# Optimization experiments

Hardware: AMD Instinct MI355X
Metric: run time of the kernel (lower is better)

Reference implementation:

```python
import jax, jax.numpy as jnp
import numpy as np

HID = 256; NH = 8; DH = 32; NL = 2
NV = 20000; NT = 50000; NE = 100000; NC = 8; FIN = 64


def setup_inputs() -> dict:
    ks = jax.random.split(jax.random.key(0), 32)
    f = lambda i, sh, s: jax.random.normal(ks[i], sh, dtype=jnp.float32) * s
    return {
        "x_v": f(0, (NV, FIN), 1.0),
        "x_t": f(1, (NT, FIN), 1.0),
        "ei_vt_src": jax.random.randint(ks[2], (NE,), 0, NV),
        "ei_vt_dst": jax.random.randint(ks[3], (NE,), 0, NT),
        "ei_tv_src": jax.random.randint(ks[4], (NE,), 0, NT),
        "ei_tv_dst": jax.random.randint(ks[5], (NE,), 0, NV),
        "ei_tt_src": jax.random.randint(ks[6], (NE,), 0, NT),
        "ei_tt_dst": jax.random.randint(ks[7], (NE,), 0, NT),
        "current": jax.random.randint(ks[8], (NC, 2), 0, NV),
        "W_in_v": f(9, (FIN, HID), 0.05), "b_in_v": jnp.zeros((HID,)),
        "W_in_t": f(10, (FIN, HID), 0.05), "b_in_t": jnp.zeros((HID,)),
        "Wk": f(11, (NL, 2, HID, HID), 0.05), "bk": jnp.zeros((NL, 2, HID)),
        "Wq": f(12, (NL, 2, HID, HID), 0.05), "bq": jnp.zeros((NL, 2, HID)),
        "Wv": f(13, (NL, 2, HID, HID), 0.05), "bv": jnp.zeros((NL, 2, HID)),
        "Wa": f(14, (NL, 2, HID, HID), 0.05), "ba": jnp.zeros((NL, 2, HID)),
        "skip": jnp.zeros((NL, 2)),
        "a_rel": f(15, (NL, 3, NH, DH, DH), 0.1),
        "m_rel": f(16, (NL, 3, NH, DH, DH), 0.1),
        "p_rel": jnp.ones((NL, 3, NH)),
        "Ws1": f(17, (2 * HID, HID), 0.05), "bs1": jnp.zeros((HID,)),
        "Ws2": f(18, (HID, 2), 0.05), "bs2": jnp.zeros((2,)),
    }


def reference(x_v, x_t, ei_vt_src, ei_vt_dst, ei_tv_src, ei_tv_dst,
              ei_tt_src, ei_tt_dst, current,
              W_in_v, b_in_v, W_in_t, b_in_t,
              Wk, bk, Wq, bq, Wv, bv, Wa, ba, skip,
              a_rel, m_rel, p_rel, Ws1, bs1, Ws2, bs2):
    scale = 1.0 / jnp.sqrt(jnp.float32(DH))
    # input projections + relu (lin_dict)
    hv = jax.nn.relu(x_v @ W_in_v + b_in_v)
    ht = jax.nn.relu(x_t @ W_in_t + b_in_t)
    # edge types: (src_type, dst_type, rel_idx, src_idx, dst_idx); 0=vehicle, 1=track
    edges = [(0, 1, 0, ei_vt_src, ei_vt_dst),
             (1, 0, 1, ei_tv_src, ei_tv_dst),
             (1, 1, 2, ei_tt_src, ei_tt_dst)]
    for l in range(NL):
        h = (hv, ht)
        proj = lambda W, b, t: (h[t] @ W[l, t] + b[l, t]).reshape(-1, NH, DH)
        k = (proj(Wk, bk, 0), proj(Wk, bk, 1))
        q = (proj(Wq, bq, 0), proj(Wq, bq, 1))
        v = (proj(Wv, bv, 0), proj(Wv, bv, 1))
        agg = [jnp.zeros((NV, NH, DH), jnp.float32),
               jnp.zeros((NT, NH, DH), jnp.float32)]
        for (st, dt, r, si, di) in edges:
            nd = agg[dt].shape[0]
            ke = jnp.einsum('ehd,hdf->ehf', k[st][si], a_rel[l, r])  # [E,H,D]
            ve = jnp.einsum('ehd,hdf->ehf', v[st][si], m_rel[l, r])  # [E,H,D]
            logit = (q[dt][di] * ke).sum(-1) * p_rel[l, r] * scale    # [E,H]
            m = jax.ops.segment_max(logit, di, num_segments=nd)
            e = jnp.exp(logit - m[di])
            s = jax.ops.segment_sum(e, di, num_segments=nd)
            alpha = e / (s[di] + 1e-16)
            agg[dt] = agg[dt] + jax.ops.segment_sum(alpha[..., None] * ve, di,
                                                    num_segments=nd)
        new = []
        for t in (0, 1):
            o = jax.nn.gelu(agg[t].reshape(-1, HID), approximate=False) @ Wa[l, t] + ba[l, t]
            beta = jax.nn.sigmoid(skip[l, t])
            new.append(beta * o + (1.0 - beta) * h[t])
        hv, ht = new
    # batched Scorer over (current vehicles) x (all tracks); cat([track, vehicle])
    veh = hv[current[:, 0]]                 # [C,HID]
    tpart = ht @ Ws1[:HID]                  # [NT,HID]
    vpart = veh @ Ws1[HID:] + bs1           # [C,HID]
    hmid = jax.nn.relu(tpart[None, :, :] + vpart[:, None, :])  # [C,NT,HID]
    out = hmid @ Ws2 + bs2                  # [C,NT,2]
    return out[..., 0], jax.nn.sigmoid(out[..., 1])
```

## Files before the change

kernel.cpp:

```cpp
#include <hip/hip_runtime.h>
#include <hip/hip_bf16.h>
#include <math.h>

#define HID 256
#define NH 8
#define DH 32
#define NL 2
#define NV 20000
#define NT 50000
#define NE 100000
#define NC 8
#define FIN 64

typedef unsigned short u16;
typedef unsigned int u32;
typedef short s16x8 __attribute__((ext_vector_type(8)));
typedef float f32x4 __attribute__((ext_vector_type(4)));

__device__ __forceinline__ float bf2f(u16 u) { return __uint_as_float(((u32)u) << 16); }
__device__ __forceinline__ u16 f2bf(float f) {
    u32 x = __float_as_uint(f);
    u32 r = ((x >> 16) & 1u) + 0x7fffu;
    return (u16)((x + r) >> 16);
}
__device__ __forceinline__ void up2(u32 u, float& a, float& b) {
    a = __uint_as_float(u << 16);
    b = __uint_as_float(u & 0xffff0000u);
}
__device__ __forceinline__ s16x8 gelu8(s16x8 a) {
    s16x8 r;
#pragma unroll
    for (int i = 0; i < 8; i++) {
        float v = bf2f((u16)a[i]);
        v = 0.5f * v * (1.f + erff(v * 0.70710678118654752f));
        r[i] = (short)f2bf(v);
    }
    return r;
}

__global__ void k_zero_i(int* __restrict__ p, int n) {
    for (int i = blockIdx.x * 256 + threadIdx.x; i < n; i += gridDim.x * 256) p[i] = 0;
}

__global__ void k_hist3(const int* __restrict__ d0, const int* __restrict__ d1, const int* __restrict__ d2,
                        int* __restrict__ cnt3) {
    int r = blockIdx.x >> 9;
    int b = blockIdx.x & 511;
    const int* dst = (r == 0) ? d0 : (r == 1) ? d1 : d2;
    int* cnt = cnt3 + (size_t)r * NT;
    for (int e = b * 256 + threadIdx.x; e < NE; e += 512 * 256)
        atomicAdd(&cnt[dst[e]], 1);
}

__global__ __launch_bounds__(1024) void k_scan3(const int* __restrict__ cnt3,
                                                int* __restrict__ rp0, int* __restrict__ rp1, int* __restrict__ rp2) {
    int r = blockIdx.x;
    const int* cnt = cnt3 + (size_t)r * NT;
    int* rp = (r == 0) ? rp0 : (r == 1) ? rp1 : rp2;
    int n = (r == 1) ? NV : NT;
    __shared__ int wsum[16];
    __shared__ int carry_s;
    int t = threadIdx.x, lane = t & 63, wv = t >> 6;
    if (t == 0) { carry_s = 0; rp[0] = 0; }
    __syncthreads();
    for (int base = 0; base < n; base += 1024) {
        int v = (base + t < n) ? cnt[base + t] : 0;
        int x = v;
#pragma unroll
        for (int off = 1; off < 64; off <<= 1) {
            int y = __shfl_up(x, off, 64);
            if (lane >= off) x += y;
        }
        if (lane == 63) wsum[wv] = x;
        __syncthreads();
        if (wv == 0 && lane < 16) {
            int s = wsum[lane];
#pragma unroll
            for (int off = 1; off < 16; off <<= 1) {
                int y = __shfl_up(s, off, 64);
                if (lane >= off) s += y;
            }
            wsum[lane] = s;
        }
        __syncthreads();
        int prefix = carry_s + (wv > 0 ? wsum[wv - 1] : 0);
        if (base + t < n) rp[base + t + 1] = prefix + x;
        __syncthreads();
        if (t == 0) carry_s += wsum[15];
        __syncthreads();
    }
}

__global__ void k_copy3(const int* __restrict__ rp0, const int* __restrict__ rp1, const int* __restrict__ rp2,
                        int* __restrict__ fill3) {
    int r = blockIdx.x >> 8;
    int b = blockIdx.x & 255;
    const int* rp = (r == 0) ? rp0 : (r == 1) ? rp1 : rp2;
    int n = (r == 1) ? NV : NT;
    int* fill = fill3 + (size_t)r * NT;
    for (int i = b * 256 + threadIdx.x; i < n; i += 256 * 256) fill[i] = rp[i];
}

__global__ void k_scatter3(const int* __restrict__ d0, const int* __restrict__ s0,
                           const int* __restrict__ d1, const int* __restrict__ s1,
                           const int* __restrict__ d2, const int* __restrict__ s2,
                           int* __restrict__ fill3,
                           int* __restrict__ es0, int* __restrict__ es1, int* __restrict__ es2) {
    int r = blockIdx.x >> 9;
    int b = blockIdx.x & 511;
    const int* dst = (r == 0) ? d0 : (r == 1) ? d1 : d2;
    const int* src = (r == 0) ? s0 : (r == 1) ? s1 : s2;
    int* fill = fill3 + (size_t)r * NT;
    int* es = (r == 0) ? es0 : (r == 1) ? es1 : es2;
    for (int e = b * 256 + threadIdx.x; e < NE; e += 512 * 256) {
        int d = dst[e];
        int p = atomicAdd(&fill[d], 1);
        es[p] = src[e];
    }
}

__global__ __launch_bounds__(256) void k_in_proj(const float* __restrict__ X, const float* __restrict__ W,
                          const float* __restrict__ b, u16* __restrict__ Y, int N) {
    const int NPB = 16;
    __shared__ float xs[NPB][FIN];
    int n0 = blockIdx.x * NPB;
    int t = threadIdx.x;
    for (int idx = t; idx < NPB * FIN; idx += 256) {
        int i = idx >> 6, c = idx & 63;
        int n = n0 + i;
        xs[i][c] = (n < N) ? X[(size_t)n * FIN + c] : 0.f;
    }
    __syncthreads();
    float acc[NPB];
#pragma unroll
    for (int i = 0; i < NPB; i++) acc[i] = 0.f;
    for (int c = 0; c < FIN; c++) {
        float w = W[c * HID + t];
#pragma unroll
        for (int i = 0; i < NPB; i++) acc[i] += xs[i][c] * w;
    }
    float bb = b[t];
    for (int i = 0; i < NPB; i++) {
        int n = n0 + i;
        if (n < N) Y[(size_t)n * HID + t] = f2bf(fmaxf(acc[i] + bb, 0.f));
    }
}

__device__ __forceinline__ int swz_idx(int k, int n) {
    int ks = k >> 5, r = k & 31;
    int j = r & 7;
    int l = ((r >> 3) << 4) | (n & 15);
    int nt = n >> 4;
    return ((ks * 16 + nt) * 64 + l) * 8 + j;
}

__global__ __launch_bounds__(256) void k_fuse_w2(
        const float* __restrict__ Wk_, const float* __restrict__ bk_, const float* __restrict__ Rk,
        u16* __restrict__ WswK, float* __restrict__ bkO,
        const float* __restrict__ Wv_, const float* __restrict__ bv_, const float* __restrict__ Rv,
        u16* __restrict__ WswV, float* __restrict__ bvO) {
    int h = blockIdx.x & 7;
    int which = blockIdx.x >> 3;
    const float* W = which ? Wv_ : Wk_;
    const float* b = which ? bv_ : bk_;
    const float* R = which ? Rv : Rk;
    u16* Wsw = which ? WswV : WswK;
    float* bout = which ? bvO : bkO;
    __shared__ float sR[DH * DH];
    int t = threadIdx.x;
    for (int idx = t; idx < DH * DH; idx += 256) sR[idx] = R[h * DH * DH + idx];
    __syncthreads();
    int f = t & 31, c0 = t >> 5;
    for (int c = c0; c < HID; c += 8) {
        float acc = 0.f;
#pragma unroll
        for (int d = 0; d < DH; d++) acc += W[c * HID + h * DH + d] * sR[d * DH + f];
        Wsw[swz_idx(c, h * DH + f)] = f2bf(acc);
    }
    if (t < DH) {
        float acc = 0.f;
#pragma unroll
        for (int d = 0; d < DH; d++) acc += b[h * DH + d] * sR[d * DH + t];
        bout[h * DH + t] = acc;
    }
}

__global__ __launch_bounds__(256) void k_swz_multi(const float* __restrict__ Wq, const float* __restrict__ Wa,
                                                   const float* __restrict__ Ws1, u16* __restrict__ out) {
    int slot = blockIdx.x >> 8;
    int idx = ((blockIdx.x & 255) << 8) | threadIdx.x;
    const float* src = (slot < 4) ? (Wq + (size_t)slot * 65536)
                     : (slot < 8) ? (Wa + (size_t)(slot - 4) * 65536)
                                  : Ws1;
    int j = idx & 7, l = (idx >> 3) & 63, nt = (idx >> 9) & 15, ks = idx >> 13;
    int k = ks * 32 + (l >> 4) * 8 + j;
    int n = nt * 16 + (l & 15);
    out[(size_t)slot * 65536 + idx] = f2bf(src[k * HID + n]);
}

template <int MODE, int GELU>
__global__ __launch_bounds__(256) void k_mm(const u16* __restrict__ X, const u16* __restrict__ Wsw,
                                            const float* __restrict__ bias, void* __restrict__ Y,
                                            const float* __restrict__ skip_, int N) {
    int tid = threadIdx.x;
    int w = tid >> 6, lane = tid & 63;
    int r0 = blockIdx.x * 16;
    int rA = r0 + (lane & 15);
    int koffg = lane >> 4;
    s16x8 a[8];
    if (rA < N) {
        const s16x8* ap = (const s16x8*)(X + (size_t)rA * HID) + koffg;
#pragma unroll
        for (int ks = 0; ks < 8; ks++) a[ks] = ap[ks * 4];
    } else {
#pragma unroll
        for (int ks = 0; ks < 8; ks++) a[ks] = (s16x8){0, 0, 0, 0, 0, 0, 0, 0};
    }
    if (GELU) {
#pragma unroll
        for (int ks = 0; ks < 8; ks++) a[ks] = gelu8(a[ks]);
    }
    f32x4 acc[4];
#pragma unroll
    for (int nt = 0; nt < 4; nt++) acc[nt] = (f32x4){0.f, 0.f, 0.f, 0.f};
    const s16x8* wp = (const s16x8*)Wsw;
#pragma unroll
    for (int ks = 0; ks < 8; ks++) {
        const s16x8* wq = wp + (size_t)ks * 16 * 64 + lane;
#pragma unroll
        for (int nt = 0; nt < 4; nt++) {
            s16x8 b = wq[(w * 4 + nt) * 64];
            acc[nt] = __builtin_amdgcn_mfma_f32_16x16x32_bf16(a[ks], b, acc[nt], 0, 0, 0);
        }
    }
    int colb = lane & 15;
    int rowb = r0 + koffg * 4;
    float beta = 0.f, ombeta = 0.f;
    if (MODE == 2) { beta = 1.f / (1.f + expf(-skip_[0])); ombeta = 1.f - beta; }
#pragma unroll
    for (int nt = 0; nt < 4; nt++) {
        int col = w * 64 + nt * 16 + colb;
        float bb = (MODE == 1 || MODE == 3) ? 0.f : bias[col];
#pragma unroll
        for (int j = 0; j < 4; j++) {
            int row = rowb + j;
            if (row < N) {
                float v = acc[nt][j] + bb;
                if (MODE == 0 || MODE == 3) {
                    ((u16*)Y)[(size_t)row * HID + col] = f2bf(v);
                } else if (MODE == 1) {
                    ((float*)Y)[(size_t)row * HID + col] = v;
                } else {
                    u16* hp = (u16*)Y + (size_t)row * HID + col;
                    *hp = f2bf(beta * v + ombeta * bf2f(*hp));
                }
            }
        }
    }
}

__global__ __launch_bounds__(256) void k_mm_gt(const u16* __restrict__ agg, const u16* __restrict__ WaSw,
                                               const float* __restrict__ ba_, const float* __restrict__ skip_,
                                               const u16* __restrict__ ht_old, const u16* __restrict__ Ws1Sw,
                                               u16* __restrict__ tpart, int N) {
    __shared__ u16 sH[16][264];
    int tid = threadIdx.x;
    int w = tid >> 6, lane = tid & 63;
    int r0 = blockIdx.x * 16;
    int rA = r0 + (lane & 15);
    int koffg = lane >> 4;
    s16x8 a[8];
    {
        const s16x8* ap = (const s16x8*)(agg + (size_t)rA * HID) + koffg;
#pragma unroll
        for (int ks = 0; ks < 8; ks++) a[ks] = gelu8(ap[ks * 4]);
    }
    f32x4 acc[4];
#pragma unroll
    for (int nt = 0; nt < 4; nt++) acc[nt] = (f32x4){0.f, 0.f, 0.f, 0.f};
    const s16x8* wp = (const s16x8*)WaSw;
#pragma unroll
    for (int ks = 0; ks < 8; ks++) {
        const s16x8* wq = wp + (size_t)ks * 16 * 64 + lane;
#pragma unroll
        for (int nt = 0; nt < 4; nt++)
            acc[nt] = __builtin_amdgcn_mfma_f32_16x16x32_bf16(a[ks], wq[(w * 4 + nt) * 64], acc[nt], 0, 0, 0);
    }
    float beta = 1.f / (1.f + expf(-skip_[0])), ombeta = 1.f - beta;
    int colb = lane & 15;
    int rowl = koffg * 4;
#pragma unroll
    for (int nt = 0; nt < 4; nt++) {
        int col = w * 64 + nt * 16 + colb;
        float bb = ba_[col];
#pragma unroll
        for (int j = 0; j < 4; j++) {
            int row = r0 + rowl + j;
            float v = acc[nt][j] + bb;
            float o = beta * v + ombeta * bf2f(ht_old[(size_t)row * HID + col]);
            sH[rowl + j][col] = f2bf(o);
        }
    }
    __syncthreads();
    s16x8 a2[8];
#pragma unroll
    for (int ks = 0; ks < 8; ks++)
        a2[ks] = *(const s16x8*)&sH[lane & 15][ks * 32 + koffg * 8];
#pragma unroll
    for (int nt = 0; nt < 4; nt++) acc[nt] = (f32x4){0.f, 0.f, 0.f, 0.f};
    const s16x8* wp2 = (const s16x8*)Ws1Sw;
#pragma unroll
    for (int ks = 0; ks < 8; ks++) {
        const s16x8* wq = wp2 + (size_t)ks * 16 * 64 + lane;
#pragma unroll
        for (int nt = 0; nt < 4; nt++)
            acc[nt] = __builtin_amdgcn_mfma_f32_16x16x32_bf16(a2[ks], wq[(w * 4 + nt) * 64], acc[nt], 0, 0, 0);
    }
#pragma unroll
    for (int nt = 0; nt < 4; nt++) {
        int col = w * 64 + nt * 16 + colb;
#pragma unroll
        for (int j = 0; j < 4; j++) {
            int row = r0 + rowl + j;
            if (row < N) tpart[(size_t)row * HID + col] = f2bf(acc[nt][j]);
        }
    }
}

__global__ __launch_bounds__(256) void k_mm2(const u16* __restrict__ X,
                                             const u16* __restrict__ W1, const float* __restrict__ b1, u16* __restrict__ Y1,
                                             const u16* __restrict__ W2, const float* __restrict__ b2, u16* __restrict__ Y2,
                                             int N) {
    int tid = threadIdx.x;
    int w = tid >> 6, lane = tid & 63;
    int r0 = blockIdx.x * 16;
    int rA = r0 + (lane & 15);
    int koffg = lane >> 4;
    s16x8 a[8];
    if (rA < N) {
        const s16x8* ap = (const s16x8*)(X + (size_t)rA * HID) + koffg;
#pragma unroll
        for (int ks = 0; ks < 8; ks++) a[ks] = ap[ks * 4];
    } else {
#pragma unroll
        for (int ks = 0; ks < 8; ks++) a[ks] = (s16x8){0, 0, 0, 0, 0, 0, 0, 0};
    }
    int colb = lane & 15;
    int rowb = r0 + koffg * 4;
#pragma unroll
    for (int pass = 0; pass < 2; pass++) {
        const u16* Wsw = pass ? W2 : W1;
        const float* bias = pass ? b2 : b1;
        u16* Y = pass ? Y2 : Y1;
        f32x4 acc[4];
#pragma unroll
        for (int nt = 0; nt < 4; nt++) acc[nt] = (f32x4){0.f, 0.f, 0.f, 0.f};
        const s16x8* wp = (const s16x8*)Wsw;
#pragma unroll
        for (int ks = 0; ks < 8; ks++) {
            const s16x8* wq = wp + (size_t)ks * 16 * 64 + lane;
#pragma unroll
            for (int nt = 0; nt < 4; nt++) {
                s16x8 b = wq[(w * 4 + nt) * 64];
                acc[nt] = __builtin_amdgcn_mfma_f32_16x16x32_bf16(a[ks], b, acc[nt], 0, 0, 0);
            }
        }
#pragma unroll
        for (int nt = 0; nt < 4; nt++) {
            int col = w * 64 + nt * 16 + colb;
            float bb = bias[col];
#pragma unroll
            for (int j = 0; j < 4; j++) {
                int row = rowb + j;
                if (row < N) Y[(size_t)row * HID + col] = f2bf(acc[nt][j] + bb);
            }
        }
    }
}

__global__ __launch_bounds__(256) void k_mm3(const u16* __restrict__ X,
                                             const u16* __restrict__ W0, const float* __restrict__ b0, u16* __restrict__ Y0,
                                             const u16* __restrict__ W1, const float* __restrict__ b1, u16* __restrict__ Y1,
                                             const u16* __restrict__ W2, const float* __restrict__ b2, u16* __restrict__ Y2,
                                             int N) {
    int tid = threadIdx.x;
    int w = tid >> 6, lane = tid & 63;
    int r0 = blockIdx.x * 16;
    int rA = r0 + (lane & 15);
    int koffg = lane >> 4;
    s16x8 a[8];
    if (rA < N) {
        const s16x8* ap = (const s16x8*)(X + (size_t)rA * HID) + koffg;
#pragma unroll
        for (int ks = 0; ks < 8; ks++) a[ks] = ap[ks * 4];
    } else {
#pragma unroll
        for (int ks = 0; ks < 8; ks++) a[ks] = (s16x8){0, 0, 0, 0, 0, 0, 0, 0};
    }
    int colb = lane & 15;
    int rowb = r0 + koffg * 4;
#pragma unroll
    for (int pass = 0; pass < 3; pass++) {
        const u16* Wsw = (pass == 0) ? W0 : (pass == 1) ? W1 : W2;
        const float* bias = (pass == 0) ? b0 : (pass == 1) ? b1 : b2;
        u16* Y = (pass == 0) ? Y0 : (pass == 1) ? Y1 : Y2;
        f32x4 acc[4];
#pragma unroll
        for (int nt = 0; nt < 4; nt++) acc[nt] = (f32x4){0.f, 0.f, 0.f, 0.f};
        const s16x8* wp = (const s16x8*)Wsw;
#pragma unroll
        for (int ks = 0; ks < 8; ks++) {
            const s16x8* wq = wp + (size_t)ks * 16 * 64 + lane;
#pragma unroll
            for (int nt = 0; nt < 4; nt++) {
                s16x8 b = wq[(w * 4 + nt) * 64];
                acc[nt] = __builtin_amdgcn_mfma_f32_16x16x32_bf16(a[ks], b, acc[nt], 0, 0, 0);
            }
        }
#pragma unroll
        for (int nt = 0; nt < 4; nt++) {
            int col = w * 64 + nt * 16 + colb;
            float bb = bias[col];
#pragma unroll
            for (int j = 0; j < 4; j++) {
                int row = rowb + j;
                if (row < N) Y[(size_t)row * HID + col] = f2bf(acc[nt][j] + bb);
            }
        }
    }
}

__device__ __forceinline__ void attn_pass(const u16* __restrict__ kA, const u16* __restrict__ vM,
                                          const int* __restrict__ es, int jb, int je,
                                          float q0, float q1, float q2, float q3, float ph, int lane4,
                                          float& o0, float& o1, float& o2, float& o3) {
    float m = -INFINITY, ss = 0.f, a0 = 0.f, a1 = 0.f, a2 = 0.f, a3 = 0.f;
    uint2 ku0 = {0, 0}, vu0 = {0, 0}, ku1 = {0, 0}, vu1 = {0, 0};
    if (jb < je) {
        int s = es[jb];
        ku0 = *(const uint2*)(kA + (size_t)s * HID + lane4);
        vu0 = *(const uint2*)(vM + (size_t)s * HID + lane4);
    }
    if (jb + 1 < je) {
        int s = es[jb + 1];
        ku1 = *(const uint2*)(kA + (size_t)s * HID + lane4);
        vu1 = *(const uint2*)(vM + (size_t)s * HID + lane4);
    }
    for (int j = jb; j < je; j++) {
        uint2 ku = ku0, vu = vu0;
        ku0 = ku1; vu0 = vu1;
        if (j + 2 < je) {
            int s = es[j + 2];
            ku1 = *(const uint2*)(kA + (size_t)s * HID + lane4);
            vu1 = *(const uint2*)(vM + (size_t)s * HID + lane4);
        }
        float k0, k1, k2, k3; up2(ku.x, k0, k1); up2(ku.y, k2, k3);
        float part = q0 * k0 + q1 * k1 + q2 * k2 + q3 * k3;
        part += __shfl_xor(part, 1, 64);
        part += __shfl_xor(part, 2, 64);
        part += __shfl_xor(part, 4, 64);
        float logit = part * ph;
        float nm = fmaxf(m, logit);
        float corr = expf(m - nm);
        float ee = expf(logit - nm);
        float v0, v1, v2, v3; up2(vu.x, v0, v1); up2(vu.y, v2, v3);
        ss = ss * corr + ee;
        a0 = a0 * corr + ee * v0; a1 = a1 * corr + ee * v1;
        a2 = a2 * corr + ee * v2; a3 = a3 * corr + ee * v3;
        m = nm;
    }
    float inv = 1.f / (ss + 1e-16f);
    o0 += a0 * inv; o1 += a1 * inv; o2 += a2 * inv; o3 += a3 * inv;
}

__global__ __launch_bounds__(256) void k_node_attn(
        const u16* __restrict__ q, const u16* __restrict__ kA, const u16* __restrict__ vM,
        const int* __restrict__ rp, const int* __restrict__ es,
        const float* __restrict__ P, float scale,
        u16* __restrict__ agg, int Nd) {
    int node = blockIdx.x * 4 + (threadIdx.x >> 6);
    if (node >= Nd) return;
    int lane = threadIdx.x & 63;
    float ph = P[lane >> 3] * scale;
    uint2 qu = *(const uint2*)(q + (size_t)node * HID + lane * 4);
    float q0, q1, q2, q3; up2(qu.x, q0, q1); up2(qu.y, q2, q3);
    float o0 = 0.f, o1 = 0.f, o2 = 0.f, o3 = 0.f;
    attn_pass(kA, vM, es, rp[node], rp[node + 1], q0, q1, q2, q3, ph, lane * 4, o0, o1, o2, o3);
    u16* ap = agg + (size_t)node * HID + lane * 4;
    ap[0] = f2bf(o0); ap[1] = f2bf(o1); ap[2] = f2bf(o2); ap[3] = f2bf(o3);
}

__global__ __launch_bounds__(256) void k_attn8(
        const u16* __restrict__ q8, const u16* __restrict__ kA, const u16* __restrict__ vM,
        const int* __restrict__ rp, const int* __restrict__ es, const int* __restrict__ current,
        const float* __restrict__ P, float scale, u16* __restrict__ agg8) {
    int wv = blockIdx.x * 4 + (threadIdx.x >> 6);
    if (wv >= NC) return;
    int node = current[wv * 2];
    int lane = threadIdx.x & 63;
    int lane4 = lane * 4;
    float ph = P[lane >> 3] * scale;
    uint2 qu = *(const uint2*)(q8 + (size_t)wv * HID + lane4);
    float q0, q1, q2, q3; up2(qu.x, q0, q1); up2(qu.y, q2, q3);
    float o0 = 0.f, o1 = 0.f, o2 = 0.f, o3 = 0.f;
    attn_pass(kA, vM, es, rp[node], rp[node + 1], q0, q1, q2, q3, ph, lane4, o0, o1, o2, o3);
    u16* ap = agg8 + (size_t)wv * HID + lane4;
    ap[0] = f2bf(o0); ap[1] = f2bf(o1); ap[2] = f2bf(o2); ap[3] = f2bf(o3);
}

__global__ __launch_bounds__(256) void k_q8(const u16* __restrict__ hv, const int* __restrict__ current,
                                            const float* __restrict__ Wq_, const float* __restrict__ bq_,
                                            u16* __restrict__ q8) {
    __shared__ float row[HID];
    int t = threadIdx.x;
    for (int c = 0; c < NC; c++) {
        int n = current[c * 2];
        row[t] = bf2f(hv[(size_t)n * HID + t]);
        __syncthreads();
        float acc = 0.f;
        for (int i = 0; i < HID; i++) acc += row[i] * Wq_[i * HID + t];
        q8[c * HID + t] = f2bf(acc + bq_[t]);
        __syncthreads();
    }
}

__global__ __launch_bounds__(256) void k_node_attn2(
        const u16* __restrict__ q,
        const u16* __restrict__ kA0, const u16* __restrict__ vM0,
        const int* __restrict__ rp0, const int* __restrict__ es0, const float* __restrict__ P0,
        const u16* __restrict__ kA1, const u16* __restrict__ vM1,
        const int* __restrict__ rp1, const int* __restrict__ es1, const float* __restrict__ P1,
        float scale, u16* __restrict__ agg, int Nd) {
    int node = blockIdx.x * 4 + (threadIdx.x >> 6);
    if (node >= Nd) return;
    int lane = threadIdx.x & 63;
    int h = lane >> 3;
    int lane4 = lane * 4;
    float ph0 = P0[h] * scale, ph1 = P1[h] * scale;
    uint2 qu = *(const uint2*)(q + (size_t)node * HID + lane4);
    float q0, q1, q2, q3; up2(qu.x, q0, q1); up2(qu.y, q2, q3);
    float o0 = 0.f, o1 = 0.f, o2 = 0.f, o3 = 0.f;
    attn_pass(kA0, vM0, es0, rp0[node], rp0[node + 1], q0, q1, q2, q3, ph0, lane4, o0, o1, o2, o3);
    attn_pass(kA1, vM1, es1, rp1[node], rp1[node + 1], q0, q1, q2, q3, ph1, lane4, o0, o1, o2, o3);
    u16* ap = agg + (size_t)node * HID + lane4;
    ap[0] = f2bf(o0); ap[1] = f2bf(o1); ap[2] = f2bf(o2); ap[3] = f2bf(o3);
}

__global__ __launch_bounds__(256) void k_vpart_f(
        const u16* __restrict__ agg8, const float* __restrict__ Wa_, const float* __restrict__ ba_,
        const float* __restrict__ skip_, const u16* __restrict__ hv, const int* __restrict__ current,
        const float* __restrict__ Ws1, const float* __restrict__ bs1, float* __restrict__ vpart) {
    __shared__ float sG[NC][HID];
    int t = threadIdx.x;
#pragma unroll
    for (int c = 0; c < NC; c++) {
        float x = bf2f(agg8[c * HID + t]);
        sG[c][t] = 0.5f * x * (1.f + erff(x * 0.70710678118654752f));
    }
    __syncthreads();
    float acc[NC];
#pragma unroll
    for (int c = 0; c < NC; c++) acc[c] = 0.f;
    for (int i = 0; i < HID; i++) {
        float wv_ = Wa_[i * HID + t];
#pragma unroll
        for (int c = 0; c < NC; c++) acc[c] += sG[c][i] * wv_;
    }
    float beta = 1.f / (1.f + expf(-skip_[0])), ombeta = 1.f - beta;
    float bb = ba_[t];
    __syncthreads();
#pragma unroll
    for (int c = 0; c < NC; c++) {
        int n = current[c * 2];
        float o = beta * (acc[c] + bb) + ombeta * bf2f(hv[(size_t)n * HID + t]);
        sG[c][t] = bf2f(f2bf(o));
    }
    __syncthreads();
    float acc2[NC];
#pragma unroll
    for (int c = 0; c < NC; c++) acc2[c] = 0.f;
    for (int i = 0; i < HID; i++) {
        float w1 = Ws1[(size_t)(HID + i) * HID + t];
#pragma unroll
        for (int c = 0; c < NC; c++) acc2[c] += sG[c][i] * w1;
    }
    float bs = bs1[t];
#pragma unroll
    for (int c = 0; c < NC; c++) vpart[c * HID + t] = acc2[c] + bs;
}

__global__ __launch_bounds__(256) void k_final(const u16* __restrict__ tpart, const float* __restrict__ vpart,
                        const float* __restrict__ Ws2, const float* __restrict__ bs2,
                        float* __restrict__ out) {
    __shared__ float vp[NC * HID];
    int t = threadIdx.x;
    for (int idx = t; idx < NC * HID; idx += 256) vp[idx] = vpart[idx];
    __syncthreads();
    int lane = t & 63, w = t >> 6;
    float w20[4], w21[4];
#pragma unroll
    for (int i = 0; i < 4; i++) {
        w20[i] = Ws2[(lane + 64 * i) * 2 + 0];
        w21[i] = Ws2[(lane + 64 * i) * 2 + 1];
    }
    float b0 = bs2[0], b1 = bs2[1];
    for (int n = blockIdx.x * 4 + w; n < NT; n += gridDim.x * 4) {
        float tp[4];
#pragma unroll
        for (int i = 0; i < 4; i++) tp[i] = bf2f(tpart[(size_t)n * HID + lane + 64 * i]);
#pragma unroll
        for (int c = 0; c < NC; c++) {
            float a0 = 0.f, a1 = 0.f;
#pragma unroll
            for (int i = 0; i < 4; i++) {
                float hm = fmaxf(tp[i] + vp[c * HID + lane + 64 * i], 0.f);
                a0 += hm * w20[i];
                a1 += hm * w21[i];
            }
#pragma unroll
            for (int off = 32; off >= 1; off >>= 1) {
                a0 += __shfl_xor(a0, off, 64);
                a1 += __shfl_xor(a1, off, 64);
            }
            if (lane == 0) {
                out[(size_t)c * NT + n] = a0 + b0;
                float z = a1 + b1;
                out[(size_t)NC * NT + (size_t)c * NT + n] = 1.f / (1.f + expf(-z));
            }
        }
    }
}

extern "C" void kernel_launch(void* const* d_in, const int* in_sizes, int n_in,
                              void* d_out, int out_size, void* d_ws, size_t ws_size,
                              hipStream_t stream) {
    (void)in_sizes; (void)n_in; (void)out_size;
    const float* x_v    = (const float*)d_in[0];
    const float* x_t    = (const float*)d_in[1];
    const int* ei_vt_s  = (const int*)d_in[2];
    const int* ei_vt_d  = (const int*)d_in[3];
    const int* ei_tv_s  = (const int*)d_in[4];
    const int* ei_tv_d  = (const int*)d_in[5];
    const int* ei_tt_s  = (const int*)d_in[6];
    const int* ei_tt_d  = (const int*)d_in[7];
    const int* current  = (const int*)d_in[8];
    const float* W_in_v = (const float*)d_in[9];
    const float* b_in_v = (const float*)d_in[10];
    const float* W_in_t = (const float*)d_in[11];
    const float* b_in_t = (const float*)d_in[12];
    const float* Wk     = (const float*)d_in[13];
    const float* bk     = (const float*)d_in[14];
    const float* Wq     = (const float*)d_in[15];
    const float* bq     = (const float*)d_in[16];
    const float* Wv     = (const float*)d_in[17];
    const float* bv     = (const float*)d_in[18];
    const float* Wa     = (const float*)d_in[19];
    const float* ba     = (const float*)d_in[20];
    const float* skip   = (const float*)d_in[21];
    const float* a_rel  = (const float*)d_in[22];
    const float* m_rel  = (const float*)d_in[23];
    const float* p_rel  = (const float*)d_in[24];
    const float* Ws1    = (const float*)d_in[25];
    const float* bs1    = (const float*)d_in[26];
    const float* Ws2    = (const float*)d_in[27];
    const float* bs2    = (const float*)d_in[28];

    char* p = (char*)d_ws;
    auto alloc = [&](size_t bytes) -> char* {
        char* r = p;
        p += (bytes + 255) & ~(size_t)255;
        return r;
    };
    u16* hv   = (u16*)alloc((size_t)NV * HID * 2);
    u16* ht   = (u16*)alloc((size_t)NT * HID * 2);
    u16* qb   = (u16*)alloc((size_t)NT * HID * 2);
    u16* qv   = (u16*)alloc((size_t)NV * HID * 2);
    u16* kA   = (u16*)alloc((size_t)NT * HID * 2);
    u16* vM   = (u16*)alloc((size_t)NT * HID * 2);
    u16* kA0  = (u16*)alloc((size_t)NV * HID * 2);
    u16* vM0  = (u16*)alloc((size_t)NV * HID * 2);
    u16* agg  = (u16*)alloc((size_t)NT * HID * 2);
    int* rp_vt = (int*)alloc((size_t)(NT + 1) * 4);
    int* rp_tv = (int*)alloc((size_t)(NV + 1) * 4);
    int* rp_tt = (int*)alloc((size_t)(NT + 1) * 4);
    int* es_vt = (int*)alloc((size_t)NE * 4);
    int* es_tv = (int*)alloc((size_t)NE * 4);
    int* es_tt = (int*)alloc((size_t)NE * 4);
    int* cnt3  = (int*)alloc((size_t)3 * NT * 4);
    int* fill3 = (int*)alloc((size_t)3 * NT * 4);
    float* vp  = (float*)alloc((size_t)NC * HID * 4);
    u16* q8   = (u16*)alloc((size_t)NC * HID * 2);
    u16* agg8 = (u16*)alloc((size_t)NC * HID * 2);
    float* bkF = (float*)alloc(HID * 4);
    float* bvF = (float*)alloc(HID * 4);
    u16*  wswK = (u16*)alloc((size_t)HID * HID * 2);
    u16*  wswV = (u16*)alloc((size_t)HID * HID * 2);
    u16*  wswK2 = (u16*)alloc((size_t)HID * HID * 2);
    u16*  wswV2 = (u16*)alloc((size_t)HID * HID * 2);
    float* bkF2 = (float*)alloc(HID * 4);
    float* bvF2 = (float*)alloc(HID * 4);
    u16*  wswA = (u16*)alloc((size_t)9 * HID * HID * 2);
    if ((size_t)(p - (char*)d_ws) > ws_size) return;

    const float scale = 0.17677669529663687f;

    k_zero_i<<<256, 256, 0, stream>>>(cnt3, 3 * NT);
    k_hist3<<<3 * 512, 256, 0, stream>>>(ei_vt_d, ei_tv_d, ei_tt_d, cnt3);
    k_scan3<<<3, 1024, 0, stream>>>(cnt3, rp_vt, rp_tv, rp_tt);
    k_copy3<<<3 * 256, 256, 0, stream>>>(rp_vt, rp_tv, rp_tt, fill3);
    k_scatter3<<<3 * 512, 256, 0, stream>>>(ei_vt_d, ei_vt_s, ei_tv_d, ei_tv_s, ei_tt_d, ei_tt_s,
                                            fill3, es_vt, es_tv, es_tt);

    k_swz_multi<<<9 * 256, 256, 0, stream>>>(Wq, Wa, Ws1, wswA);

    k_in_proj<<<(NV + 15) / 16, 256, 0, stream>>>(x_v, W_in_v, b_in_v, hv, NV);
    k_in_proj<<<(NT + 15) / 16, 256, 0, stream>>>(x_t, W_in_t, b_in_t, ht, NT);

    const int GV = (NV + 15) / 16, GT = (NT + 15) / 16;

    for (int l = 0; l < NL; l++) {
        const float* Wk0 = Wk + (size_t)(l * 2 + 0) * HID * HID;
        const float* Wk1 = Wk + (size_t)(l * 2 + 1) * HID * HID;
        const float* bk0 = bk + (l * 2 + 0) * HID, *bk1 = bk + (l * 2 + 1) * HID;
        const float* Wv0 = Wv + (size_t)(l * 2 + 0) * HID * HID;
        const float* Wv1 = Wv + (size_t)(l * 2 + 1) * HID * HID;
        const float* bv0 = bv + (l * 2 + 0) * HID, *bv1 = bv + (l * 2 + 1) * HID;
        const float* bq0 = bq + (l * 2 + 0) * HID, *bq1 = bq + (l * 2 + 1) * HID;
        const u16* WqS0 = wswA + (size_t)(l * 2 + 0) * 65536;
        const u16* WqS1 = wswA + (size_t)(l * 2 + 1) * 65536;
        const u16* WaS0 = wswA + (size_t)(4 + l * 2 + 0) * 65536;
        const u16* WaS1 = wswA + (size_t)(4 + l * 2 + 1) * 65536;
        const float* A0 = a_rel + (size_t)(l * 3 + 0) * NH * DH * DH;
        const float* A1 = a_rel + (size_t)(l * 3 + 1) * NH * DH * DH;
        const float* A2 = a_rel + (size_t)(l * 3 + 2) * NH * DH * DH;
        const float* M0 = m_rel + (size_t)(l * 3 + 0) * NH * DH * DH;
        const float* M1 = m_rel + (size_t)(l * 3 + 1) * NH * DH * DH;
        const float* M2 = m_rel + (size_t)(l * 3 + 2) * NH * DH * DH;
        const float* P0 = p_rel + (size_t)(l * 3 + 0) * NH;
        const float* P1 = p_rel + (size_t)(l * 3 + 1) * NH;
        const float* P2 = p_rel + (size_t)(l * 3 + 2) * NH;

        k_fuse_w2<<<2 * NH, 256, 0, stream>>>(Wk0, bk0, A0, wswK, bkF, Wv0, bv0, M0, wswV, bvF);
        if (l == 0) {
            k_mm3<<<GV, 256, 0, stream>>>(hv, WqS0, bq0, qv, wswK, bkF, kA0, wswV, bvF, vM0, NV);
        } else {
            k_mm2<<<GV, 256, 0, stream>>>(hv, wswK, bkF, kA0, wswV, bvF, vM0, NV);
            k_q8<<<1, 256, 0, stream>>>(hv, current, Wq + (size_t)(l * 2 + 0) * HID * HID, bq0, q8);
        }

        k_fuse_w2<<<2 * NH, 256, 0, stream>>>(Wk1, bk1, A1, wswK, bkF, Wv1, bv1, M1, wswV, bvF);
        k_mm3<<<GT, 256, 0, stream>>>(ht, WqS1, bq1, qb, wswK, bkF, kA, wswV, bvF, vM, NT);

        if (l == 0) {
            k_node_attn<<<(NV + 3) / 4, 256, 0, stream>>>(qv, kA, vM, rp_tv, es_tv, P1, scale, agg, NV);
            k_mm<2, 1><<<GV, 256, 0, stream>>>(agg, WaS0, ba + (l * 2 + 0) * HID, hv, skip + (l * 2 + 0), NV);
        } else {
            k_attn8<<<2, 256, 0, stream>>>(q8, kA, vM, rp_tv, es_tv, current, P1, scale, agg8);
        }

        k_fuse_w2<<<2 * NH, 256, 0, stream>>>(Wk1, bk1, A2, wswK2, bkF2, Wv1, bv1, M2, wswV2, bvF2);
        k_mm2<<<GT, 256, 0, stream>>>(ht, wswK2, bkF2, kA, wswV2, bvF2, vM, NT);

        k_node_attn2<<<(NT + 3) / 4, 256, 0, stream>>>(qb, kA0, vM0, rp_vt, es_vt, P0,
                                                       kA, vM, rp_tt, es_tt, P2, scale, agg, NT);

        if (l == 0) {
            k_mm<2, 1><<<GT, 256, 0, stream>>>(agg, WaS1, ba + (l * 2 + 1) * HID, ht, skip + (l * 2 + 1), NT);
        } else {
            k_mm_gt<<<GT, 256, 0, stream>>>(agg, WaS1, ba + (l * 2 + 1) * HID, skip + (l * 2 + 1),
                                            ht, wswA + (size_t)8 * 65536, kA, NT);
        }
    }

    k_vpart_f<<<1, 256, 0, stream>>>(agg8, Wa + (size_t)2 * 65536, ba + 2 * HID, skip + 2,
                                     hv, current, Ws1, bs1, vp);
    k_final<<<2048, 256, 0, stream>>>(kA , vp, Ws2, bs2, (float*)d_out);
}
```

Before: 976.9 us.

## Fuse layer-0 vehicle output projection with layer-1 K/V projection

Unrolls the layer loop and adds a kernel that applies GELU, the Wa output projection and the skip blend to the vehicle aggregate. It then reuses the updated hidden rows from shared memory to compute the next layer's K and V projections. The layer-0 vehicle attention writes into the q buffer in place, and its output projection is deferred so it merges with the layer-1 K/V matmul. This removes one kernel launch and one global round trip of hv. The risk is that reusing the qv buffer for aggregates and reordering the launches changes data dependencies.

```diff
diff --git a/kernel.cpp b/kernel.cpp
--- a/kernel.cpp
+++ b/kernel.cpp
@@ -323,6 +323,84 @@
         for (int j = 0; j < 4; j++) {
             int row = r0 + rowl + j;
             if (row < N) tpart[(size_t)row * HID + col] = f2bf(acc[nt][j]);
+        }
+    }
+}
+
+__global__ __launch_bounds__(256) void k_mm_dv(const u16* __restrict__ aggv, const u16* __restrict__ WaSw,
+                                               const float* __restrict__ ba_, const float* __restrict__ skip_,
+                                               u16* __restrict__ hv,
+                                               const u16* __restrict__ WkSw, const float* __restrict__ bkF,
+                                               const u16* __restrict__ WvSw, const float* __restrict__ bvF,
+                                               u16* __restrict__ kA0, u16* __restrict__ vM0, int N) {
+    __shared__ u16 sH[16][264];
+    int tid = threadIdx.x;
+    int w = tid >> 6, lane = tid & 63;
+    int r0 = blockIdx.x * 16;
+    int rA = r0 + (lane & 15);
+    int koffg = lane >> 4;
+    s16x8 a[8];
+    {
+        const s16x8* ap = (const s16x8*)(aggv + (size_t)rA * HID) + koffg;
+#pragma unroll
+        for (int ks = 0; ks < 8; ks++) a[ks] = gelu8(ap[ks * 4]);
+    }
+    f32x4 acc[4];
+#pragma unroll
+    for (int nt = 0; nt < 4; nt++) acc[nt] = (f32x4){0.f, 0.f, 0.f, 0.f};
+    const s16x8* wp = (const s16x8*)WaSw;
+#pragma unroll
+    for (int ks = 0; ks < 8; ks++) {
+        const s16x8* wq = wp + (size_t)ks * 16 * 64 + lane;
+#pragma unroll
+        for (int nt = 0; nt < 4; nt++)
+            acc[nt] = __builtin_amdgcn_mfma_f32_16x16x32_bf16(a[ks], wq[(w * 4 + nt) * 64], acc[nt], 0, 0, 0);
+    }
+    float beta = 1.f / (1.f + expf(-skip_[0])), ombeta = 1.f - beta;
+    int colb = lane & 15;
+    int rowl = koffg * 4;
+#pragma unroll
+    for (int nt = 0; nt < 4; nt++) {
+        int col = w * 64 + nt * 16 + colb;
+        float bb = ba_[col];
+#pragma unroll
+        for (int j = 0; j < 4; j++) {
+            int row = r0 + rowl + j;
+            float v = acc[nt][j] + bb;
+            u16 o = f2bf(beta * v + ombeta * bf2f(hv[(size_t)row * HID + col]));
+            hv[(size_t)row * HID + col] = o;
+            sH[rowl + j][col] = o;
+        }
+    }
+    __syncthreads();
+    s16x8 a2[8];
+#pragma unroll
+    for (int ks = 0; ks < 8; ks++)
+        a2[ks] = *(const s16x8*)&sH[lane & 15][ks * 32 + koffg * 8];
+#pragma unroll
+    for (int pass = 0; pass < 2; pass++) {
+        const u16* Wsw = pass ? WvSw : WkSw;
+        const float* bias = pass ? bvF : bkF;
+        u16* Y = pass ? vM0 : kA0;
+#pragma unroll
+        for (int nt = 0; nt < 4; nt++) acc[nt] = (f32x4){0.f, 0.f, 0.f, 0.f};
+        const s16x8* wp2 = (const s16x8*)Wsw;
+#pragma unroll
+        for (int ks = 0; ks < 8; ks++) {
+            const s16x8* wq = wp2 + (size_t)ks * 16 * 64 + lane;
+#pragma unroll
+            for (int nt = 0; nt < 4; nt++)
+                acc[nt] = __builtin_amdgcn_mfma_f32_16x16x32_bf16(a2[ks], wq[(w * 4 + nt) * 64], acc[nt], 0, 0, 0);
+        }
+#pragma unroll
+        for (int nt = 0; nt < 4; nt++) {
+            int col = w * 64 + nt * 16 + colb;
+            float bb = bias[col];
+#pragma unroll
+            for (int j = 0; j < 4; j++) {
+                int row = r0 + rowl + j;
+                if (row < N) Y[(size_t)row * HID + col] = f2bf(acc[nt][j] + bb);
+            }
         }
     }
 }
@@ -710,67 +788,47 @@
     k_copy3<<<3 * 256, 256, 0, stream>>>(rp_vt, rp_tv, rp_tt, fill3);
     k_scatter3<<<3 * 512, 256, 0, stream>>>(ei_vt_d, ei_vt_s, ei_tv_d, ei_tv_s, ei_tt_d, ei_tt_s,
                                             fill3, es_vt, es_tv, es_tt);
-
     k_swz_multi<<<9 * 256, 256, 0, stream>>>(Wq, Wa, Ws1, wswA);
-
     k_in_proj<<<(NV + 15) / 16, 256, 0, stream>>>(x_v, W_in_v, b_in_v, hv, NV);
     k_in_proj<<<(NT + 15) / 16, 256, 0, stream>>>(x_t, W_in_t, b_in_t, ht, NT);
 
     const int GV = (NV + 15) / 16, GT = (NT + 15) / 16;
-
-    for (int l = 0; l < NL; l++) {
-        const float* Wk0 = Wk + (size_t)(l * 2 + 0) * HID * HID;
-        const float* Wk1 = Wk + (size_t)(l * 2 + 1) * HID * HID;
-        const float* bk0 = bk + (l * 2 + 0) * HID, *bk1 = bk + (l * 2 + 1) * HID;
-        const float* Wv0 = Wv + (size_t)(l * 2 + 0) * HID * HID;
-        const float* Wv1 = Wv + (size_t)(l * 2 + 1) * HID * HID;
-        const float* bv0 = bv + (l * 2 + 0) * HID, *bv1 = bv + (l * 2 + 1) * HID;
-        const float* bq0 = bq + (l * 2 + 0) * HID, *bq1 = bq + (l * 2 + 1) * HID;
-        const u16* WqS0 = wswA + (size_t)(l * 2 + 0) * 65536;
-        const u16* WqS1 = wswA + (size_t)(l * 2 + 1) * 65536;
-        const u16* WaS0 = wswA + (size_t)(4 + l * 2 + 0) * 65536;
-        const u16* WaS1 = wswA + (size_t)(4 + l * 2 + 1) * 65536;
-        const float* A0 = a_rel + (size_t)(l * 3 + 0) * NH * DH * DH;
-        const float* A1 = a_rel + (size_t)(l * 3 + 1) * NH * DH * DH;
-        const float* A2 = a_rel + (size_t)(l * 3 + 2) * NH * DH * DH;
-        const float* M0 = m_rel + (size_t)(l * 3 + 0) * NH * DH * DH;
-        const float* M1 = m_rel + (size_t)(l * 3 + 1) * NH * DH * DH;
-        const float* M2 = m_rel + (size_t)(l * 3 + 2) * NH * DH * DH;
-        const float* P0 = p_rel + (size_t)(l * 3 + 0) * NH;
-        const float* P1 = p_rel + (size_t)(l * 3 + 1) * NH;
-        const float* P2 = p_rel + (size_t)(l * 3 + 2) * NH;
-
-        k_fuse_w2<<<2 * NH, 256, 0, stream>>>(Wk0, bk0, A0, wswK, bkF, Wv0, bv0, M0, wswV, bvF);
-        if (l == 0) {
-            k_mm3<<<GV, 256, 0, stream>>>(hv, WqS0, bq0, qv, wswK, bkF, kA0, wswV, bvF, vM0, NV);
-        } else {
-            k_mm2<<<GV, 256, 0, stream>>>(hv, wswK, bkF, kA0, wswV, bvF, vM0, NV);
-            k_q8<<<1, 256, 0, stream>>>(hv, current, Wq + (size_t)(l * 2 + 0) * HID * HID, bq0, q8);
-        }
-
-        k_fuse_w2<<<2 * NH, 256, 0, stream>>>(Wk1, bk1, A1, wswK, bkF, Wv1, bv1, M1, wswV, bvF);
-        k_mm3<<<GT, 256, 0, stream>>>(ht, WqS1, bq1, qb, wswK, bkF, kA, wswV, bvF, vM, NT);
-
-        if (l == 0) {
-            k_node_attn<<<(NV + 3) / 4, 256, 0, stream>>>(qv, kA, vM, rp_tv, es_tv, P1, scale, agg, NV);
-            k_mm<2, 1><<<GV, 256, 0, stream>>>(agg, WaS0, ba + (l * 2 + 0) * HID, hv, skip + (l * 2 + 0), NV);
-        } else {
-            k_attn8<<<2, 256, 0, stream>>>(q8, kA, vM, rp_tv, es_tv, current, P1, scale, agg8);
-        }
-
-        k_fuse_w2<<<2 * NH, 256, 0, stream>>>(Wk1, bk1, A2, wswK2, bkF2, Wv1, bv1, M2, wswV2, bvF2);
-        k_mm2<<<GT, 256, 0, stream>>>(ht, wswK2, bkF2, kA, wswV2, bvF2, vM, NT);
-
-        k_node_attn2<<<(NT + 3) / 4, 256, 0, stream>>>(qb, kA0, vM0, rp_vt, es_vt, P0,
-                                                       kA, vM, rp_tt, es_tt, P2, scale, agg, NT);
-
-        if (l == 0) {
-            k_mm<2, 1><<<GT, 256, 0, stream>>>(agg, WaS1, ba + (l * 2 + 1) * HID, ht, skip + (l * 2 + 1), NT);
-        } else {
-            k_mm_gt<<<GT, 256, 0, stream>>>(agg, WaS1, ba + (l * 2 + 1) * HID, skip + (l * 2 + 1),
-                                            ht, wswA + (size_t)8 * 65536, kA, NT);
-        }
-    }
+    const float* AR = a_rel; const float* MR = m_rel;
+#define REL_W(l, r) (AR + (size_t)((l) * 3 + (r)) * NH * DH * DH)
+#define REL_M(l, r) (MR + (size_t)((l) * 3 + (r)) * NH * DH * DH)
+#define REL_P(l, r) (p_rel + (size_t)((l) * 3 + (r)) * NH)
+
+    k_fuse_w2<<<2 * NH, 256, 0, stream>>>(Wk + 0 * 65536, bk + 0 * HID, REL_W(0, 0), wswK, bkF,
+                                          Wv + 0 * 65536, bv + 0 * HID, REL_M(0, 0), wswV, bvF);
+    k_mm3<<<GV, 256, 0, stream>>>(hv, wswA + 0 * 65536, bq + 0 * HID, qv, wswK, bkF, kA0, wswV, bvF, vM0, NV);
+    k_fuse_w2<<<2 * NH, 256, 0, stream>>>(Wk + 1 * 65536, bk + 1 * HID, REL_W(0, 1), wswK, bkF,
+                                          Wv + 1 * 65536, bv + 1 * HID, REL_M(0, 1), wswV, bvF);
+    k_mm3<<<GT, 256, 0, stream>>>(ht, wswA + 1 * 65536, bq + 1 * HID, qb, wswK, bkF, kA, wswV, bvF, vM, NT);
+    k_node_attn<<<(NV + 3) / 4, 256, 0, stream>>>(qv, kA, vM, rp_tv, es_tv, REL_P(0, 1), scale, qv, NV);
+    k_fuse_w2<<<2 * NH, 256, 0, stream>>>(Wk + 1 * 65536, bk + 1 * HID, REL_W(0, 2), wswK2, bkF2,
+                                          Wv + 1 * 65536, bv + 1 * HID, REL_M(0, 2), wswV2, bvF2);
+    k_mm2<<<GT, 256, 0, stream>>>(ht, wswK2, bkF2, kA, wswV2, bvF2, vM, NT);
+    k_node_attn2<<<(NT + 3) / 4, 256, 0, stream>>>(qb, kA0, vM0, rp_vt, es_vt, REL_P(0, 0),
+                                                   kA, vM, rp_tt, es_tt, REL_P(0, 2), scale, agg, NT);
+    k_mm<2, 1><<<GT, 256, 0, stream>>>(agg, wswA + (size_t)(4 + 1) * 65536, ba + 1 * HID, ht, skip + 1, NT);
+
+    k_fuse_w2<<<2 * NH, 256, 0, stream>>>(Wk + 2 * 65536, bk + 2 * HID, REL_W(1, 0), wswK, bkF,
+                                          Wv + 2 * 65536, bv + 2 * HID, REL_M(1, 0), wswV, bvF);
+    k_mm_dv<<<GV, 256, 0, stream>>>(qv , wswA + (size_t)(4 + 0) * 65536, ba + 0 * HID, skip + 0,
+                                    hv, wswK, bkF, wswV, bvF, kA0, vM0, NV);
+    k_q8<<<1, 256, 0, stream>>>(hv, current, Wq + (size_t)2 * 65536, bq + 2 * HID, q8);
+
+    k_fuse_w2<<<2 * NH, 256, 0, stream>>>(Wk + 3 * 65536, bk + 3 * HID, REL_W(1, 1), wswK, bkF,
+                                          Wv + 3 * 65536, bv + 3 * HID, REL_M(1, 1), wswV, bvF);
+    k_mm3<<<GT, 256, 0, stream>>>(ht, wswA + 3 * 65536, bq + 3 * HID, qb, wswK, bkF, kA, wswV, bvF, vM, NT);
+    k_attn8<<<2, 256, 0, stream>>>(q8, kA, vM, rp_tv, es_tv, current, REL_P(1, 1), scale, agg8);
+    k_fuse_w2<<<2 * NH, 256, 0, stream>>>(Wk + 3 * 65536, bk + 3 * HID, REL_W(1, 2), wswK2, bkF2,
+                                          Wv + 3 * 65536, bv + 3 * HID, REL_M(1, 2), wswV2, bvF2);
+    k_mm2<<<GT, 256, 0, stream>>>(ht, wswK2, bkF2, kA, wswV2, bvF2, vM, NT);
+    k_node_attn2<<<(NT + 3) / 4, 256, 0, stream>>>(qb, kA0, vM0, rp_vt, es_vt, REL_P(1, 0),
+                                                   kA, vM, rp_tt, es_tt, REL_P(1, 2), scale, agg, NT);
+    k_mm_gt<<<GT, 256, 0, stream>>>(agg, wswA + (size_t)(4 + 3) * 65536, ba + 3 * HID, skip + 3,
+                                    ht, wswA + (size_t)8 * 65536, kA, NT);
 
     k_vpart_f<<<1, 256, 0, stream>>>(agg8, Wa + (size_t)2 * 65536, ba + 2 * HID, skip + 2,
                                      hv, current, Ws1, bs1, vp);
```

After: 971.9 us. About the same (-0.5%).
